# Kernel optimization log

Hardware: AMD Instinct MI355X
Metric: run time of the kernel (lower is better)

The kernel has to match this reference:

```python
import jax, jax.numpy as jnp
import numpy as np

LN_EPS = 1e-5


def _layernorm_c(x, g, b):
    # x: (B, C, H, W); LayerNorm over channel dim (torch permutes to channels-last)
    m = x.mean(axis=1, keepdims=True)
    v = ((x - m) ** 2).mean(axis=1, keepdims=True)
    xn = (x - m) / jnp.sqrt(v + LN_EPS)
    return xn * g[None, :, None, None] + b[None, :, None, None]


def _conv1x1(x, w, b):
    # w: (O, C) equivalent of Conv2d kernel_size=1
    return jnp.einsum('oc,bchw->bohw', w, x) + b[None, :, None, None]


def _rel_indices(lw):
    # matches torch: indices (x,y) for x in range(lw) for y in range(lw);
    # torch indexes the (2*lw-1, 2*lw-1) table with NEGATIVE distances (python wrap),
    # which equals modulo (2*lw-1).
    pos = np.stack(np.meshgrid(np.arange(lw), np.arange(lw), indexing='ij'), -1).reshape(-1, 2)
    rel = (pos[None, :, :] - pos[:, None, :]) % (2 * lw - 1)
    return rel[..., 0], rel[..., 1]


def setup_inputs() -> dict:
    key = jax.random.key(0)
    ks = jax.random.split(key, 8)
    B, N, D, H, DFF, LW = 1, 240, 256, 8, 2048, 20
    src = jax.random.normal(ks[0], (B, D, N, N), dtype=jnp.float32)
    valid = 220  # last window block fully padded -> exercises full-mask reset path
    pad1d = jnp.arange(N) >= valid
    padding_mask = (pad1d[:, None] | pad1d[None, :])[None, None]  # (B,1,N,N) bool
    s = 0.02
    return {
        'src': src,
        'padding_mask': padding_mask,
        'qkv_w': jax.random.normal(ks[1], (3 * D, D), dtype=jnp.float32) * s,
        'qkv_b': jnp.zeros((3 * D,), jnp.float32),
        'out_w': jax.random.normal(ks[2], (D, D), dtype=jnp.float32) * s,
        'out_b': jnp.zeros((D,), jnp.float32),
        'lin1_w': jax.random.normal(ks[3], (DFF, D), dtype=jnp.float32) * s,
        'lin1_b': jnp.zeros((DFF,), jnp.float32),
        'lin2_w': jax.random.normal(ks[4], (D, DFF), dtype=jnp.float32) * s,
        'lin2_b': jnp.zeros((D,), jnp.float32),
        'n1_g': jnp.ones((D,), jnp.float32),
        'n1_b': jnp.zeros((D,), jnp.float32),
        'n2_g': jnp.ones((D,), jnp.float32),
        'n2_b': jnp.zeros((D,), jnp.float32),
        'rel_bias': jax.random.normal(ks[5], (2 * LW - 1, 2 * LW - 1, H), dtype=jnp.float32) * 0.02,
    }


def reference(src, padding_mask, qkv_w, qkv_b, out_w, out_b, lin1_w, lin1_b,
              lin2_w, lin2_b, n1_g, n1_b, n2_g, n2_b, rel_bias):
    B, D, N, _ = src.shape
    H = rel_bias.shape[-1]
    LW = (rel_bias.shape[0] + 1) // 2
    nw = N // LW           # shift_offset=0, N % LW == 0 -> no spatial padding
    F = LW * LW            # eff_attn_field
    hd = D // H
    scaling = float(hd) ** -0.5

    # pre-norm
    src2 = _layernorm_c(src, n1_g, n1_b)

    # window partition: (B,D,N,N) -> (B*nw*nw, D, LW, LW)
    pm = src2.reshape(B, D, nw, LW, nw, LW).transpose(0, 2, 4, 1, 3, 5)
    pm = pm.reshape(B * nw * nw, D, LW, LW)

    # key padding mask per window: (B*nw*nw, F)
    kpm = padding_mask[:, 0].reshape(B, nw, LW, nw, LW).transpose(0, 1, 3, 2, 4)
    kpm = kpm.reshape(B * nw * nw, F)
    full = kpm.all(axis=-1)                      # fully padded windows
    kpm = kpm & (~full)[:, None]                 # index_fill_(False) equivalent

    # qkv (1x1 conv) + heads
    qkv = _conv1x1(pm, qkv_w, qkv_b)             # (eb, 3D, LW, LW)
    q, k, v = jnp.split(qkv, 3, axis=1)
    eb = q.shape[0]
    q = (q * scaling).reshape(eb, H, hd, F)
    k = k.reshape(eb, H, hd, F)
    v = v.reshape(eb, H, hd, F)

    attn = jnp.einsum('bhdi,bhdj->bhij', q, k)   # (eb, H, F, F)
    attn = jnp.where(kpm[:, None, None, :], -jnp.inf, attn)
    r0, r1 = _rel_indices(LW)
    rel = rel_bias[r0, r1]                       # (F, F, H)
    attn = attn + jnp.transpose(rel, (2, 0, 1))[None]
    attn = jax.nn.softmax(attn, axis=-1)

    out = jnp.einsum('bhij,bhdj->bhdi', attn, v).reshape(eb, D, LW, LW)
    out = _conv1x1(out, out_w, out_b)

    # window merge: (B*nw*nw, D, LW, LW) -> (B, D, N, N)
    out = out.reshape(B, nw, nw, D, LW, LW).transpose(0, 3, 1, 4, 2, 5).reshape(B, D, N, N)

    src = src + out  # dropout1 = identity (eval)

    # FFN
    s2 = _layernorm_c(src, n2_g, n2_b)
    s2 = _conv1x1(jax.nn.relu(_conv1x1(s2, lin1_w, lin1_b)), lin2_w, lin2_b)
    src = src + s2   # dropout2 = identity (eval)

    src = jnp.where(padding_mask, 0.0, src)
    return src
```

## Files before the change

kernel.cpp:

```cpp
#include <hip/hip_runtime.h>
#include <hip/hip_bf16.h>
#include <math.h>

typedef unsigned short u16;
typedef unsigned int   u32;
typedef __attribute__((ext_vector_type(8))) short bf16x8;
typedef __attribute__((ext_vector_type(4))) float f32x4;
typedef __attribute__((ext_vector_type(16))) float f32x16;
typedef __attribute__((ext_vector_type(4))) u32 u32x4;

#define NSIDE  240
#define NPIX   57600
#define DMODEL 256
#define NHEAD  8
#define HDIM   32
#define LWIN   20
#define NWIN   12
#define FF     400
#define DFFN   2048
#define BTAB   39
#define LOG2E  1.4426950408889634f
#define QSCALE 0.2550773933046f

#define OFF_QKVW  0u
#define OFF_OUTW  393216u
#define OFF_W1    524288u
#define OFF_W2    1572864u
#define OFF_FLAG  2621440u
#define OFF_WANY  2621504u
#define OFF_WMASK 2622080u
#define OFF_NM    2629568u
#define OFF_A     2687488u
#define OFF_B     32178688u

__device__ __forceinline__ float bf2f(u16 u){
  union { float f; u32 i; } v; v.i = ((u32)u) << 16; return v.f;
}
__device__ __forceinline__ float bflo(u32 u){
  union { float f; u32 i; } v; v.i = u << 16; return v.f;
}
__device__ __forceinline__ float bfhi(u32 u){
  union { float f; u32 i; } v; v.i = u & 0xffff0000u; return v.f;
}
__device__ __forceinline__ u16 f2bf(float f){
  union { float f; u32 i; } v; v.f = f;
  u32 r = v.i + 0x7fffu + ((v.i >> 16) & 1u);
  return (u16)(r >> 16);
}
__device__ __forceinline__ u32 pkbf(float a, float b){
  float2 f2; f2.x = a; f2.y = b;
  __hip_bfloat162 h = __float22bfloat162_rn(f2);
  union { __hip_bfloat162 h; u32 u; } c; c.h = h; return c.u;
}
__device__ __forceinline__ void gload16(const void* g, void* l){
  __builtin_amdgcn_global_load_lds((const __attribute__((address_space(1))) u32*)g,
                                   (__attribute__((address_space(3))) u32*)l, 16, 0, 0);
}
__device__ __forceinline__ void gload16nt(const void* g, void* l){
  __builtin_amdgcn_global_load_lds((const __attribute__((address_space(1))) u32*)g,
                                   (__attribute__((address_space(3))) u32*)l, 16, 0, 2);
}

__global__ void cvt_kernel(const float* __restrict__ in, u16* __restrict__ out, int n){
  int i = blockIdx.x * 256 + threadIdx.x;
  if (i < n) out[i] = f2bf(in[i]);
}
__global__ void cvt_w1T(const float* __restrict__ in, u16* __restrict__ out){
  int i = blockIdx.x * 256 + threadIdx.x;
  int f = i >> 8, k = i & 255;
  int lane = (f & 15) | (((k >> 3) & 3) << 4);
  size_t dst = ((size_t)((f >> 4) * 8 + (k >> 5)) * 64 + lane) * 8 + (k & 7);
  out[dst] = f2bf(in[i]);
}
__global__ void cvt_w2T(const float* __restrict__ in, u16* __restrict__ out){
  int i = blockIdx.x * 256 + threadIdx.x;
  int o = i >> 11, f = i & 2047;
  int lane = (o & 15) | (((f >> 3) & 3) << 4);
  size_t dst = ((size_t)((o >> 4) * 64 + (f >> 5)) * 64 + lane) * 8 + (f & 7);
  out[dst] = f2bf(in[i]);
}

__global__ void zero_flag(int* __restrict__ flag){ *flag = 0; }
__global__ void detect_mask(const unsigned char* __restrict__ m, int* __restrict__ flag){
  int p = blockIdx.x * 256 + threadIdx.x;
  int i = p / NSIDE, j = p - i * NSIDE;
  int a = (m[p] != 0), b = (m[j * NSIDE + i] != 0);
  unsigned long long ball = __ballot(a != b);
  if ((threadIdx.x & 63) == 0 && ball) atomicOr(flag, 1);
}
__global__ void norm_mask(const void* __restrict__ m, const int* __restrict__ flag,
                          unsigned char* __restrict__ nm){
  int p = blockIdx.x * 256 + threadIdx.x;
  int v;
  if (*flag) v = (((const int*)m)[p] != 0);
  else       v = (((const unsigned char*)m)[p] != 0);
  nm[p] = (unsigned char)v;
}

__global__ void wmask_kernel(const unsigned char* __restrict__ nm,
                             u32* __restrict__ wmask, int* __restrict__ wany){
  int w = blockIdx.x;
  int wi = w / NWIN, wj = w % NWIN;
  __shared__ u32 bits[13];
  __shared__ int cnt;
  int t = threadIdx.x;
  if (t < 13) bits[t] = 0;
  if (t == 0) cnt = 0;
  __syncthreads();
  if (t < FF){
    int pj = (wi * LWIN + t / LWIN) * NSIDE + wj * LWIN + (t % LWIN);
    if (nm[pj]){ atomicOr(&bits[t >> 5], 1u << (t & 31)); atomicAdd(&cnt, 1); }
  }
  __syncthreads();
  int full = (cnt == FF);
  if (t < 13) wmask[w * 13 + t] = full ? 0u : bits[t];
  if (t == 0) wany[w] = (cnt > 0 && !full) ? 1 : 0;
}

__global__ void bias_prep(const float* __restrict__ relb, u16* __restrict__ biasT){
  int tile = blockIdx.x;
  int h = blockIdx.y;
  int it = tile / 13, jt = tile % 13;
  int t = threadIdx.x;
  int lane = t & 63, rq = t >> 6;
  int lane31 = lane & 31, hi = lane >> 5;
  int i = it * 32 + lane31; if (i > FF - 1) i = FF - 1;
  int xi = i / LWIN, yi = i % LWIN;
  u16* dst = biasT + ((size_t)(h * 169 + tile) * 64 + lane) * 16;
  #pragma unroll
  for (int q = 0; q < 4; q++){
    int r = rq * 4 + q;
    int j = jt * 32 + (r & 3) + 8 * (r >> 2) + 4 * hi;
    float v;
    if (j < FF){
      int xj = j / LWIN, yj = j % LWIN;
      int r0 = xj - xi; if (r0 < 0) r0 += BTAB;
      int r1 = yj - yi; if (r1 < 0) r1 += BTAB;
      v = LOG2E * relb[(r0 * BTAB + r1) * NHEAD + h];
    } else v = -1e30f;
    dst[r] = f2bf(v);
  }
}

__global__ __launch_bounds__(256) void ln_kernel(const float* __restrict__ x,
                          const float* __restrict__ g, const float* __restrict__ b,
                          u16* __restrict__ out){
  int p = blockIdx.x * 256 + threadIdx.x;
  float s = 0.f, s2 = 0.f;
  for (int c = 0; c < DMODEL; c++){
    float v = x[c * NPIX + p];
    s += v; s2 += v * v;
  }
  float m = s * (1.f / DMODEL);
  float var = s2 * (1.f / DMODEL) - m * m;
  float inv = rsqrtf(var + 1e-5f);
  u16* orow = out + (size_t)p * DMODEL;
  for (int c0 = 0; c0 < DMODEL; c0 += 8){
    u32 wq[4];
    #pragma unroll
    for (int q = 0; q < 4; q++){
      int c = c0 + 2 * q;
      float v0 = (x[c * NPIX + p] - m) * inv * g[c] + b[c];
      float v1 = (x[(c + 1) * NPIX + p] - m) * inv * g[c + 1] + b[c + 1];
      wq[q] = pkbf(v0, v1);
    }
    uint4 st; st.x = wq[0]; st.y = wq[1]; st.z = wq[2]; st.w = wq[3];
    *(uint4*)&orow[c0] = st;
  }
}

template<int EPI, int XHM>
__global__ __launch_bounds__(256) void gemm_nt(const u16* __restrict__ W,
    const u16* __restrict__ Xt, const float* __restrict__ bias,
    const float* __restrict__ res, void* __restrict__ outp, int M){
  __shared__ u16 SM[128 * 128];
  u16* Ws = SM;
  u16* Xs = SM + 8192;
  int t = threadIdx.x, wv = t >> 6, ln = t & 63;
  int n0 = blockIdx.x * 128, m0 = blockIdx.y * 128;
  int wr = wv >> 1, wc = wv & 1;
  f32x4 acc[4][4];
  #pragma unroll
  for (int r = 0; r < 4; r++)
    #pragma unroll
    for (int c = 0; c < 4; c++) acc[r][c] = (f32x4)0.f;
  const char* Wb = (const char*)W;
  const char* Xb = (const char*)Xt;
  for (int k0 = 0; k0 < 256; k0 += 64){
    #pragma unroll
    for (int i = 0; i < 4; i++){
      int cb = i * 256 + wv * 64;
      int idx = cb + ln;
      int row = idx >> 3, cc = idx & 7;
      int cc2 = cc ^ (row & 7);
      gload16(Wb + (size_t)(m0 + row) * 512 + k0 * 2 + (cc2 << 4), (char*)Ws + cb * 16);
      if (XHM){
        int head = (k0 >> 5) + (cc2 >> 2);
        gload16(Xb + ((size_t)head * NPIX + n0 + row) * 64 + ((cc2 & 3) << 4),
                (char*)Xs + cb * 16);
      } else {
        gload16(Xb + (size_t)(n0 + row) * 512 + k0 * 2 + (cc2 << 4), (char*)Xs + cb * 16);
      }
    }
    __syncthreads();
    #pragma unroll
    for (int kk = 0; kk < 64; kk += 32){
      int kidx = kk + (ln >> 4) * 8;
      int swz = (ln & 7) << 3;
      bf16x8 af[4], bfr[4];
      #pragma unroll
      for (int r = 0; r < 4; r++){
        int row = wr * 64 + r * 16 + (ln & 15);
        af[r] = *(const bf16x8*)&Ws[row * 64 + (kidx ^ swz)];
      }
      #pragma unroll
      for (int c = 0; c < 4; c++){
        int row = wc * 64 + c * 16 + (ln & 15);
        bfr[c] = *(const bf16x8*)&Xs[row * 64 + (kidx ^ swz)];
      }
      #pragma unroll
      for (int r = 0; r < 4; r++)
        #pragma unroll
        for (int c = 0; c < 4; c++)
          acc[r][c] = __builtin_amdgcn_mfma_f32_16x16x32_bf16(af[r], bfr[c], acc[r][c], 0, 0, 0);
    }
    __syncthreads();
  }
  if (EPI == 2){
    float sc = (m0 < 256) ? QSCALE : 1.0f;
    #pragma unroll
    for (int r = 0; r < 4; r++){
      int mo0 = wr * 64 + r * 16 + (ln >> 4) * 4;
      f32x4 bv = *(const f32x4*)&bias[m0 + mo0];
      #pragma unroll
      for (int c = 0; c < 4; c++){
        int no = wc * 64 + c * 16 + (ln & 15);
        uint2 pk;
        pk.x = pkbf((acc[r][c][0] + bv[0]) * sc, (acc[r][c][1] + bv[1]) * sc);
        pk.y = pkbf((acc[r][c][2] + bv[2]) * sc, (acc[r][c][3] + bv[3]) * sc);
        *(uint2*)&SM[no * 128 + mo0] = pk;
      }
    }
    __syncthreads();
    u16* ob = (u16*)outp;
    int plane8 = (m0 >> 8) * 8 + ((m0 & 255) >> 5);
    #pragma unroll
    for (int it = 0; it < 8; it++){
      int idx = t + it * 256;
      int pr = idx >> 4, ch = idx & 15;
      int hl = ch >> 2;
      int off = (ch & 3) * 8;
      uint4 v = *(const uint4*)&SM[pr * 128 + ch * 8];
      *(uint4*)&ob[((size_t)(plane8 + hl) * NPIX + n0 + pr) * 32 + off] = v;
    }
  } else {
    #pragma unroll
    for (int r = 0; r < 4; r++){
      int mo0 = m0 + wr * 64 + r * 16 + (ln >> 4) * 4;
      f32x4 bv = *(const f32x4*)&bias[mo0];
      #pragma unroll
      for (int c = 0; c < 4; c++){
        int no = n0 + wc * 64 + c * 16 + (ln & 15);
        #pragma unroll
        for (int q = 0; q < 4; q++){
          float v = acc[r][c][q] + bv[q];
          size_t oi = (size_t)(mo0 + q) * NPIX + no;
          ((float*)outp)[oi] = v + res[oi];
        }
      }
    }
  }
}

__global__ __launch_bounds__(256, 3) void attn_kernel(
    const u16* __restrict__ qkvP, const u16* __restrict__ biasT,
    const u32* __restrict__ wmask, const int* __restrict__ wany,
    u16* __restrict__ out)
{
  __shared__ u16 Ks[400 * 32];
  __shared__ u16 Vs[32 * 420];
  int bid = blockIdx.x;
  int xcd = bid & 7, s = bid >> 3;
  int h = ((xcd >> 1) << 1) | (s & 1);
  int w = ((s >> 1) << 1) | (xcd & 1);
  int wi = w / NWIN, wj = w % NWIN;
  int t = threadIdx.x, wv = t >> 6, ln = t & 63;
  const char* kpl = (const char*)qkvP + (size_t)(8 + h) * NPIX * 64;
  const u16*  vpl = qkvP + (size_t)(16 + h) * NPIX * 32;
  const u16*  qpl = qkvP + (size_t)h * NPIX * 32;
  #pragma unroll
  for (int it = 0; it < 7; it++){
    int base = it * 256 + wv * 64;
    if (base < 1600){
      int idx = base + ln;
      int j = idx >> 2, c = idx & 3;
      int pj = (wi * LWIN + j / LWIN) * NSIDE + wj * LWIN + (j % LWIN);
      gload16nt(kpl + (size_t)pj * 64 + ((c ^ (j & 3)) << 4), (char*)Ks + base * 16);
    }
  }
  for (int it = 0; it < 7; it++){
    int idx = t + it * 256;
    int j = idx >> 2, c = idx & 3;
    if (j >= 416) break;
    int d0 = c * 8;
    if (j < FF){
      int pj = (wi * LWIN + j / LWIN) * NSIDE + wj * LWIN + (j % LWIN);
      u32x4 vv = __builtin_nontemporal_load((const u32x4*)&vpl[(size_t)pj * 32 + c * 8]);
      #pragma unroll
      for (int q = 0; q < 4; q++){
        Vs[(d0 + 2 * q) * 420 + j]     = (u16)vv[q];
        Vs[(d0 + 2 * q + 1) * 420 + j] = (u16)(vv[q] >> 16);
      }
    } else {
      #pragma unroll
      for (int q = 0; q < 4; q++){
        Vs[(d0 + 2 * q) * 420 + j]     = 0;
        Vs[(d0 + 2 * q + 1) * 420 + j] = 0;
      }
    }
  }
  __syncthreads();
  int lane31 = ln & 31, hi = ln >> 5;
  int anym = wany[w];
  for (int it8 = wv; it8 < 13; it8 += 4){
    int i = it8 * 32 + lane31;
    int ic = i < FF ? i : FF - 1;
    int pi = (wi * LWIN + ic / LWIN) * NSIDE + wj * LWIN + (ic % LWIN);
    bf16x8 qf0 = __builtin_nontemporal_load((const bf16x8*)&qpl[(size_t)pi * 32 + hi * 8]);
    bf16x8 qf1 = __builtin_nontemporal_load((const bf16x8*)&qpl[(size_t)pi * 32 + 16 + hi * 8]);
    float m = -3e38f, lsum = 0.f;
    f32x16 o;
    #pragma unroll
    for (int r = 0; r < 16; r++) o[r] = 0.f;
    const u16* btb = biasT + ((size_t)(h * 169 + it8 * 13) * 64 + ln) * 16;
    for (int jt = 0; jt < 13; jt++){
      const uint4* bt = (const uint4*)(btb + (size_t)jt * 1024);
      uint4 bw0 = bt[0], bw1 = bt[1];
      u32 bwv[8] = {bw0.x, bw0.y, bw0.z, bw0.w, bw1.x, bw1.y, bw1.z, bw1.w};
      f32x16 acc;
      #pragma unroll
      for (int e = 0; e < 8; e++){ acc[2 * e] = bflo(bwv[e]); acc[2 * e + 1] = bfhi(bwv[e]); }
      int jb0 = jt * 32 + lane31;
      int jrc = jb0 < FF ? jb0 : FF - 1;
      const char* kb = (const char*)Ks + jrc * 64;
      bf16x8 kf0 = *(const bf16x8*)(kb + ((hi ^ (jrc & 3)) << 4));
      bf16x8 kf1 = *(const bf16x8*)(kb + (((2 + hi) ^ (jrc & 3)) << 4));
      acc = __builtin_amdgcn_mfma_f32_32x32x16_bf16(kf0, qf0, acc, 0, 0, 0);
      acc = __builtin_amdgcn_mfma_f32_32x32x16_bf16(kf1, qf1, acc, 0, 0, 0);
      if (anym){
        u32 mb = wmask[w * 13 + jt];
        if (mb){
          #pragma unroll
          for (int r = 0; r < 16; r++){
            int jb = (r & 3) + 8 * (r >> 2) + 4 * hi;
            if ((mb >> jb) & 1) acc[r] = -1e30f;
          }
        }
      }
      float tm = acc[0];
      #pragma unroll
      for (int r = 1; r < 16; r++) tm = fmaxf(tm, acc[r]);
      tm = fmaxf(tm, __shfl_xor(tm, 32));
      if (tm > m + 6.f){
        float sc = exp2f(m - tm);
        lsum *= sc;
        #pragma unroll
        for (int r = 0; r < 16; r++) o[r] *= sc;
        m = tm;
      }
      float ls = 0.f;
      #pragma unroll
      for (int r = 0; r < 16; r++){ float pv = exp2f(acc[r] - m); acc[r] = pv; ls += pv; }
      lsum += ls;
      u32 x01 = pkbf(acc[0], acc[1]), x23 = pkbf(acc[2], acc[3]);
      u32 x45 = pkbf(acc[4], acc[5]), x67 = pkbf(acc[6], acc[7]);
      u32 y01 = __shfl_xor(x01, 32), y23 = __shfl_xor(x23, 32);
      u32 y45 = __shfl_xor(x45, 32), y67 = __shfl_xor(x67, 32);
      union { u32 u[4]; bf16x8 v; } f0;
      f0.u[0] = hi ? y45 : x01; f0.u[1] = hi ? y67 : x23;
      f0.u[2] = hi ? x45 : y01; f0.u[3] = hi ? x67 : y23;
      bf16x8 vf0 = *(const bf16x8*)&Vs[lane31 * 420 + jt * 32 + hi * 8];
      o = __builtin_amdgcn_mfma_f32_32x32x16_bf16(vf0, f0.v, o, 0, 0, 0);
      if (jt < 12){
        u32 x89 = pkbf(acc[8], acc[9]),   xab = pkbf(acc[10], acc[11]);
        u32 xcd2 = pkbf(acc[12], acc[13]), xef = pkbf(acc[14], acc[15]);
        u32 y89 = __shfl_xor(x89, 32), yab = __shfl_xor(xab, 32);
        u32 ycd = __shfl_xor(xcd2, 32), yef = __shfl_xor(xef, 32);
        union { u32 u[4]; bf16x8 v; } f1;
        f1.u[0] = hi ? ycd : x89; f1.u[1] = hi ? yef : xab;
        f1.u[2] = hi ? xcd2 : y89; f1.u[3] = hi ? xef : yab;
        bf16x8 vf1 = *(const bf16x8*)&Vs[lane31 * 420 + jt * 32 + 16 + hi * 8];
        o = __builtin_amdgcn_mfma_f32_32x32x16_bf16(vf1, f1.v, o, 0, 0, 0);
      }
    }
    lsum += __shfl_xor(lsum, 32);
    if (i < FF){
      float linv = 1.f / lsum;
      u16* orow = out + ((size_t)h * NPIX + pi) * 32;
      #pragma unroll
      for (int g = 0; g < 4; g++){
        int ch0 = g * 8 + hi * 4;
        uint2 st;
        st.x = pkbf(o[g * 4 + 0] * linv, o[g * 4 + 1] * linv);
        st.y = pkbf(o[g * 4 + 2] * linv, o[g * 4 + 3] * linv);
        *(uint2*)&orow[ch0] = st;
      }
    }
  }
}

__global__ __launch_bounds__(256, 3) void ffn_kernel(const u16* __restrict__ xt,
    const u16* __restrict__ w1T, const u16* __restrict__ w2T,
    const float* __restrict__ b1, const float* __restrict__ b2,
    const float* __restrict__ resid, const unsigned char* __restrict__ pmask,
    float* __restrict__ out){
  __shared__ u16 Xs[64 * 256];
  __shared__ u16 Hs[64 * 136];
  int t = threadIdx.x, wv = t >> 6, ln = t & 63;
  int q4 = ln >> 4, l15 = ln & 15;
  int p0 = blockIdx.x * 64;
  const char* xb = (const char*)xt + (size_t)p0 * 512;
  #pragma unroll
  for (int it = 0; it < 8; it++){
    int cb = it * 256 + wv * 64;
    int idx = cb + ln;
    int row = idx >> 5, cc = idx & 31;
    gload16(xb + row * 512 + ((cc << 4) ^ ((row & 7) << 4)), (char*)Xs + cb * 16);
  }
  f32x4 acc[4][4];
  #pragma unroll
  for (int r = 0; r < 4; r++)
    #pragma unroll
    for (int c = 0; c < 4; c++) acc[r][c] = (f32x4)0.f;
  int swx = (ln & 7) << 3;
  __syncthreads();
  for (int fc = 0; fc < DFFN; fc += 128){
    f32x4 ha[2][4];
    #pragma unroll
    for (int ft = 0; ft < 2; ft++)
      #pragma unroll
      for (int c = 0; c < 4; c++) ha[ft][c] = (f32x4)0.f;
    const u16* w1f = w1T + ((size_t)((fc >> 4) + wv * 2) * 8 * 64 + ln) * 8;
    #pragma unroll
    for (int kg = 0; kg < 8; kg++){
      bf16x8 aw0 = *(const bf16x8*)(w1f + (size_t)kg * 512);
      bf16x8 aw1 = *(const bf16x8*)(w1f + (size_t)(8 + kg) * 512);
      #pragma unroll
      for (int c = 0; c < 4; c++){
        int p = c * 16 + l15;
        bf16x8 bx = *(const bf16x8*)&Xs[p * 256 + ((kg * 32 + q4 * 8) ^ swx)];
        ha[0][c] = __builtin_amdgcn_mfma_f32_16x16x32_bf16(aw0, bx, ha[0][c], 0, 0, 0);
        ha[1][c] = __builtin_amdgcn_mfma_f32_16x16x32_bf16(aw1, bx, ha[1][c], 0, 0, 0);
      }
    }
    __syncthreads();
    #pragma unroll
    for (int ft = 0; ft < 2; ft++){
      int f0 = wv * 32 + ft * 16 + q4 * 4;
      f32x4 bv1 = *(const f32x4*)&b1[fc + f0];
      #pragma unroll
      for (int c = 0; c < 4; c++){
        int p = c * 16 + l15;
        uint2 pk;
        pk.x = pkbf(fmaxf(ha[ft][c][0] + bv1[0], 0.f), fmaxf(ha[ft][c][1] + bv1[1], 0.f));
        pk.y = pkbf(fmaxf(ha[ft][c][2] + bv1[2], 0.f), fmaxf(ha[ft][c][3] + bv1[3], 0.f));
        *(uint2*)&Hs[p * 136 + f0] = pk;
      }
    }
    __syncthreads();
    #pragma unroll
    for (int kk2 = 0; kk2 < 4; kk2++){
      bf16x8 a2[4], hb[4];
      #pragma unroll
      for (int r = 0; r < 4; r++)
        a2[r] = *(const bf16x8*)(w2T + ((size_t)((wv * 4 + r) * 64 + (fc >> 5) + kk2) * 64 + ln) * 8);
      #pragma unroll
      for (int c = 0; c < 4; c++)
        hb[c] = *(const bf16x8*)&Hs[(c * 16 + l15) * 136 + kk2 * 32 + q4 * 8];
      #pragma unroll
      for (int r = 0; r < 4; r++)
        #pragma unroll
        for (int c = 0; c < 4; c++)
          acc[r][c] = __builtin_amdgcn_mfma_f32_16x16x32_bf16(a2[r], hb[c], acc[r][c], 0, 0, 0);
    }
  }
  #pragma unroll
  for (int r = 0; r < 4; r++){
    int o0 = wv * 64 + r * 16 + q4 * 4;
    f32x4 bv = *(const f32x4*)&b2[o0];
    #pragma unroll
    for (int c = 0; c < 4; c++){
      int p = p0 + c * 16 + l15;
      int msk = pmask[p];
      #pragma unroll
      for (int q = 0; q < 4; q++){
        size_t oi = (size_t)(o0 + q) * NPIX + p;
        float v = acc[r][c][q] + bv[q] + resid[oi];
        out[oi] = msk ? 0.f : v;
      }
    }
  }
}

extern "C" void kernel_launch(void* const* d_in, const int* in_sizes, int n_in,
                              void* d_out, int out_size, void* d_ws, size_t ws_size,
                              hipStream_t stream){
  const float* src    = (const float*)d_in[0];
  const void*  pmraw  = d_in[1];
  const float* qkv_w  = (const float*)d_in[2];
  const float* qkv_b  = (const float*)d_in[3];
  const float* out_w  = (const float*)d_in[4];
  const float* out_b  = (const float*)d_in[5];
  const float* lin1_w = (const float*)d_in[6];
  const float* lin1_b = (const float*)d_in[7];
  const float* lin2_w = (const float*)d_in[8];
  const float* lin2_b = (const float*)d_in[9];
  const float* n1_g   = (const float*)d_in[10];
  const float* n1_b   = (const float*)d_in[11];
  const float* n2_g   = (const float*)d_in[12];
  const float* n2_b   = (const float*)d_in[13];
  const float* relb   = (const float*)d_in[14];

  char* ws = (char*)d_ws;
  u16* qkvw_bf = (u16*)(ws + OFF_QKVW);
  u16* outw_bf = (u16*)(ws + OFF_OUTW);
  u16* w1_fr   = (u16*)(ws + OFF_W1);
  u16* w2_fr   = (u16*)(ws + OFF_W2);
  int* flag    = (int*)(ws + OFF_FLAG);
  int* wany    = (int*)(ws + OFF_WANY);
  u32* wmaskp  = (u32*)(ws + OFF_WMASK);
  unsigned char* nm = (unsigned char*)(ws + OFF_NM);
  u16* bufA    = (u16*)(ws + OFF_A);
  u16* qkvP    = (u16*)(ws + OFF_B);
  float* x1    = (float*)(ws + OFF_B);
  u16* biasT   = (u16*)d_out;

  cvt_kernel<<<768,  256, 0, stream>>>(qkv_w,  qkvw_bf, 768 * 256);
  cvt_kernel<<<256,  256, 0, stream>>>(out_w,  outw_bf, 256 * 256);
  cvt_w1T<<<2048, 256, 0, stream>>>(lin1_w, w1_fr);
  cvt_w2T<<<2048, 256, 0, stream>>>(lin2_w, w2_fr);
  zero_flag<<<1, 1, 0, stream>>>(flag);
  detect_mask<<<225, 256, 0, stream>>>((const unsigned char*)pmraw, flag);
  norm_mask<<<225, 256, 0, stream>>>(pmraw, flag, nm);
  wmask_kernel<<<144, 512, 0, stream>>>(nm, wmaskp, wany);
  bias_prep<<<dim3(169, 8), 256, 0, stream>>>(relb, biasT);

  ln_kernel<<<225, 256, 0, stream>>>(src, n1_g, n1_b, bufA);
  gemm_nt<2, 0><<<dim3(450, 6), 256, 0, stream>>>(qkvw_bf, bufA, qkv_b, nullptr,
                                                  (void*)qkvP, 768);
  attn_kernel<<<1152, 256, 0, stream>>>(qkvP, biasT, wmaskp, wany, bufA);
  gemm_nt<1, 1><<<dim3(450, 2), 256, 0, stream>>>(outw_bf, bufA, out_b, src,
                                                  (void*)x1, 256);
  ln_kernel<<<225, 256, 0, stream>>>(x1, n2_g, n2_b, bufA);
  ffn_kernel<<<900, 256, 0, stream>>>(bufA, w1_fr, w2_fr, lin1_b, lin2_b, x1, nm,
                                      (float*)d_out);
}
```

Measured before the change: 640.4 us.

## Fuse relative-bias table lookup into attention kernel via shared-memory bias

Removes the separate bias_prep kernel and its precomputed bf16 bias tiles in global memory. Each attention block now loads the small 39x39 per-head bias table into shared memory and gathers the bias per score element using the query and key window coordinates. This saves a kernel launch and the per-tile global bias reads, but adds integer div/mod work and LDS gathers inside the inner loop. It also raises LDS use, lowers the occupancy hint from 3 to 2, and replaces the XCD-aware block-to-(head, window) mapping with a plain one, which may hurt L2 locality.

```diff
diff --git a/kernel.cpp b/kernel.cpp
--- a/kernel.cpp
+++ b/kernel.cpp
@@ -117,31 +117,6 @@
   if (t == 0) wany[w] = (cnt > 0 && !full) ? 1 : 0;
 }
 
-__global__ void bias_prep(const float* __restrict__ relb, u16* __restrict__ biasT){
-  int tile = blockIdx.x;
-  int h = blockIdx.y;
-  int it = tile / 13, jt = tile % 13;
-  int t = threadIdx.x;
-  int lane = t & 63, rq = t >> 6;
-  int lane31 = lane & 31, hi = lane >> 5;
-  int i = it * 32 + lane31; if (i > FF - 1) i = FF - 1;
-  int xi = i / LWIN, yi = i % LWIN;
-  u16* dst = biasT + ((size_t)(h * 169 + tile) * 64 + lane) * 16;
-  #pragma unroll
-  for (int q = 0; q < 4; q++){
-    int r = rq * 4 + q;
-    int j = jt * 32 + (r & 3) + 8 * (r >> 2) + 4 * hi;
-    float v;
-    if (j < FF){
-      int xj = j / LWIN, yj = j % LWIN;
-      int r0 = xj - xi; if (r0 < 0) r0 += BTAB;
-      int r1 = yj - yi; if (r1 < 0) r1 += BTAB;
-      v = LOG2E * relb[(r0 * BTAB + r1) * NHEAD + h];
-    } else v = -1e30f;
-    dst[r] = f2bf(v);
-  }
-}
-
 __global__ __launch_bounds__(256) void ln_kernel(const float* __restrict__ x,
                           const float* __restrict__ g, const float* __restrict__ b,
                           u16* __restrict__ out){
@@ -272,22 +247,27 @@
   }
 }
 
-__global__ __launch_bounds__(256, 3) void attn_kernel(
-    const u16* __restrict__ qkvP, const u16* __restrict__ biasT,
+__global__ __launch_bounds__(256, 2) void attn_kernel(
+    const u16* __restrict__ qkvP, const float* __restrict__ relb,
     const u32* __restrict__ wmask, const int* __restrict__ wany,
     u16* __restrict__ out)
 {
   __shared__ u16 Ks[400 * 32];
   __shared__ u16 Vs[32 * 420];
+  __shared__ float bs[BTAB * BTAB];
   int bid = blockIdx.x;
-  int xcd = bid & 7, s = bid >> 3;
-  int h = ((xcd >> 1) << 1) | (s & 1);
-  int w = ((s >> 1) << 1) | (xcd & 1);
+  int h = bid & 7, w = bid >> 3;
   int wi = w / NWIN, wj = w % NWIN;
   int t = threadIdx.x, wv = t >> 6, ln = t & 63;
   const char* kpl = (const char*)qkvP + (size_t)(8 + h) * NPIX * 64;
   const u16*  vpl = qkvP + (size_t)(16 + h) * NPIX * 32;
   const u16*  qpl = qkvP + (size_t)h * NPIX * 32;
+  for (int e = t; e < BTAB * BTAB; e += 256){
+    int a = e / BTAB, b = e - a * BTAB;
+    int r0 = a + 20; if (r0 >= BTAB) r0 -= BTAB;
+    int r1 = b + 20; if (r1 >= BTAB) r1 -= BTAB;
+    bs[e] = LOG2E * relb[(r0 * BTAB + r1) * NHEAD + h];
+  }
   #pragma unroll
   for (int it = 0; it < 7; it++){
     int base = it * 256 + wv * 64;
@@ -325,21 +305,27 @@
   for (int it8 = wv; it8 < 13; it8 += 4){
     int i = it8 * 32 + lane31;
     int ic = i < FF ? i : FF - 1;
-    int pi = (wi * LWIN + ic / LWIN) * NSIDE + wj * LWIN + (ic % LWIN);
+    int xi = ic / LWIN, yi = ic - xi * LWIN;
+    int pi = (wi * LWIN + xi) * NSIDE + wj * LWIN + yi;
+    int Coff = (19 - xi) * BTAB + (19 - yi);
     bf16x8 qf0 = __builtin_nontemporal_load((const bf16x8*)&qpl[(size_t)pi * 32 + hi * 8]);
     bf16x8 qf1 = __builtin_nontemporal_load((const bf16x8*)&qpl[(size_t)pi * 32 + 16 + hi * 8]);
     float m = -3e38f, lsum = 0.f;
     f32x16 o;
     #pragma unroll
     for (int r = 0; r < 16; r++) o[r] = 0.f;
-    const u16* btb = biasT + ((size_t)(h * 169 + it8 * 13) * 64 + ln) * 16;
     for (int jt = 0; jt < 13; jt++){
-      const uint4* bt = (const uint4*)(btb + (size_t)jt * 1024);
-      uint4 bw0 = bt[0], bw1 = bt[1];
-      u32 bwv[8] = {bw0.x, bw0.y, bw0.z, bw0.w, bw1.x, bw1.y, bw1.z, bw1.w};
       f32x16 acc;
-      #pragma unroll
-      for (int e = 0; e < 8; e++){ acc[2 * e] = bflo(bwv[e]); acc[2 * e + 1] = bfhi(bwv[e]); }
+      int jbase = jt * 32 + 4 * hi;
+      #pragma unroll
+      for (int r = 0; r < 16; r++){
+        int j = jbase + (r & 3) + 8 * (r >> 2);
+        int jc2 = j < FF ? j : 0;
+        int xj = jc2 / LWIN;
+        int yj = jc2 - xj * LWIN;
+        float bv = bs[xj * BTAB + yj + Coff];
+        acc[r] = (j < FF) ? bv : -1e30f;
+      }
       int jb0 = jt * 32 + lane31;
       int jrc = jb0 < FF ? jb0 : FF - 1;
       const char* kb = (const char*)Ks + jrc * 64;
@@ -533,7 +519,6 @@
   u16* bufA    = (u16*)(ws + OFF_A);
   u16* qkvP    = (u16*)(ws + OFF_B);
   float* x1    = (float*)(ws + OFF_B);
-  u16* biasT   = (u16*)d_out;
 
   cvt_kernel<<<768,  256, 0, stream>>>(qkv_w,  qkvw_bf, 768 * 256);
   cvt_kernel<<<256,  256, 0, stream>>>(out_w,  outw_bf, 256 * 256);
@@ -543,12 +528,11 @@
   detect_mask<<<225, 256, 0, stream>>>((const unsigned char*)pmraw, flag);
   norm_mask<<<225, 256, 0, stream>>>(pmraw, flag, nm);
   wmask_kernel<<<144, 512, 0, stream>>>(nm, wmaskp, wany);
-  bias_prep<<<dim3(169, 8), 256, 0, stream>>>(relb, biasT);
 
   ln_kernel<<<225, 256, 0, stream>>>(src, n1_g, n1_b, bufA);
   gemm_nt<2, 0><<<dim3(450, 6), 256, 0, stream>>>(qkvw_bf, bufA, qkv_b, nullptr,
                                                   (void*)qkvP, 768);
-  attn_kernel<<<1152, 256, 0, stream>>>(qkvP, biasT, wmaskp, wany, bufA);
+  attn_kernel<<<1152, 256, 0, stream>>>(qkvP, relb, wmaskp, wany, bufA);
   gemm_nt<1, 1><<<dim3(450, 2), 256, 0, stream>>>(outw_bf, bufA, out_b, src,
                                                   (void*)x1, 256);
   ln_kernel<<<225, 256, 0, stream>>>(x1, n2_g, n2_b, bufA);
```

After: 550.8 us. -14.0%, faster.
